# Performance work log

Measured on AMD Instinct MI355X. Metric: run time of the kernel, lower is better.

Reference implementation:

```python
import jax, jax.numpy as jnp
import numpy as np

B, N, C, H = 2, 2048, 1024, 16
D = C // H
EPS = 1e-5  # torch LayerNorm default


def layernorm(x, gamma, beta):
    mu = jnp.mean(x, axis=-1, keepdims=True)
    var = jnp.mean(jnp.square(x - mu), axis=-1, keepdims=True)
    return (x - mu) * jax.lax.rsqrt(var + EPS) * gamma + beta


def setup_inputs() -> dict:
    key = jax.random.key(0)
    ks = jax.random.split(key, 4)
    x = jax.random.normal(ks[0], (B, N, C), dtype=jnp.float32)
    w_qkv = jax.random.normal(ks[1], (3 * C, C), dtype=jnp.float32) * (C ** -0.5)
    w_proj = jax.random.normal(ks[2], (C, C), dtype=jnp.float32) * (C ** -0.5)
    return {
        "x": x,
        "w_qkv": w_qkv,
        "q_gamma": jnp.ones((C,), jnp.float32),
        "q_beta": jnp.zeros((C,), jnp.float32),
        "k_gamma": jnp.ones((C,), jnp.float32),
        "k_beta": jnp.zeros((C,), jnp.float32),
        "lpe_w": jnp.ones((C,), jnp.float32),
        "lpe_b": jnp.zeros((C,), jnp.float32),
        "w_proj": w_proj,
        "b_proj": jnp.zeros((C,), jnp.float32),
    }


def reference(x, w_qkv, q_gamma, q_beta, k_gamma, k_beta, lpe_w, lpe_b, w_proj, b_proj):
    b, n, c = x.shape
    scale = D ** -0.5
    qkv = jnp.einsum('bnc,fc->bnf', x, w_qkv)            # (B,N,3C)
    qkv = qkv.reshape(b, n, 3, H, D)
    q, k, v = qkv[:, :, 0], qkv[:, :, 1], qkv[:, :, 2]   # (B,N,H,D)
    # QK-norm: LayerNorm over flattened heads (dim C)
    q = layernorm(q.reshape(b, n, c), q_gamma, q_beta).reshape(b, n, H, D)
    k = layernorm(k.reshape(b, n, c), k_gamma, k_beta).reshape(b, n, H, D)
    # LPE: depthwise 1x1x1 conv == per-channel affine on v
    v_lpe = v.reshape(b, n, c) * lpe_w + lpe_b           # (B,N,C)
    # attention
    attn = jnp.einsum('bqhd,bkhd->bhqk', q * scale, k)   # (B,H,N,N)
    attn = jax.nn.softmax(attn, axis=-1)
    out = jnp.einsum('bhqk,bkhd->bqhd', attn, v).reshape(b, n, c)
    y = jnp.einsum('bnc,oc->bno', out + v_lpe, w_proj) + b_proj
    return y
```

## Files before the change

kernel.cpp:

```cpp
#include <hip/hip_runtime.h>
#include <stdint.h>

#define Bdim 2
#define Ndim 2048
#define Cdim 1024
#define Hdim 16
#define Ddim 64
#define Fdim 3072
#define Mdim 4096

typedef unsigned int  u32;
typedef unsigned short u16;
typedef float f32x4 __attribute__((ext_vector_type(4)));
typedef short s16x8 __attribute__((ext_vector_type(8)));
typedef unsigned short u16x4 __attribute__((ext_vector_type(4)));
typedef unsigned int u32x2 __attribute__((ext_vector_type(2)));

__device__ __forceinline__ u16 f2b(float f) {
  u32 u = __builtin_bit_cast(u32, f);
  u += 0x7FFFu + ((u >> 16) & 1u);
  return (u16)(u >> 16);
}
__device__ __forceinline__ float b2f(u16 h) {
  return __builtin_bit_cast(float, (u32)h << 16);
}
__device__ __forceinline__ u32 cvtpk(float a, float b) {
  u32 d;
  asm("v_cvt_pk_bf16_f32 %0, %1, %2" : "=v"(d) : "v"(a), "v"(b));
  return d;
}
__device__ __forceinline__ float rexp2(float x) { return __builtin_amdgcn_exp2f(x); }
__device__ __forceinline__ f32x4 mfma16(s16x8 a, s16x8 b, f32x4 c) {
  return __builtin_amdgcn_mfma_f32_16x16x32_bf16(a, b, c, 0, 0, 0);
}
__device__ __forceinline__ void gl_lds16(const void* g, void* l) {
  __builtin_amdgcn_global_load_lds(
      (const __attribute__((address_space(1))) void*)g,
      (__attribute__((address_space(3))) void*)l, 16, 0, 0);
}
__device__ __forceinline__ bool is_bf16(const void* qg) {
  return *(const u32*)qg == 0x3F803F80u;
}

__global__ __launch_bounds__(256)
void k_prep(const void* x, const void* wq, const void* wp,
            const void* g0, const void* g1, const void* g2, const void* g3,
            const void* g4, const void* g5, const void* g6,
            u16* xb, u16* wqb, u16* wpb, float* prm) {
  const int i = blockIdx.x * 256 + threadIdx.x;
  const bool isbf = is_bf16(g0);
  const void* src; u16* dst; int k;
  if (i < 1048576)      { src = x;  dst = xb;  k = i; }
  else if (i < 1835008) { src = wq; dst = wqb; k = i - 1048576; }
  else if (i < 2097152) { src = wp; dst = wpb; k = i - 1835008; }
  else {
    const int j = i - 2097152;
    if (j >= 1792) return;
    const int fi = j * 4;
    const int pi = fi >> 10, off = fi & 1023;
    const void* s = (pi == 0) ? g0 : (pi == 1) ? g1 : (pi == 2) ? g2
                  : (pi == 3) ? g3 : (pi == 4) ? g4 : (pi == 5) ? g5 : g6;
    float4 v;
    if (isbf) {
      u16x4 h = *(const u16x4*)((const u16*)s + off);
      v.x = b2f(h.x); v.y = b2f(h.y); v.z = b2f(h.z); v.w = b2f(h.w);
    } else {
      v = *(const float4*)((const float*)s + off);
    }
    *(float4*)(prm + fi) = v;
    return;
  }
  if (isbf) {
    ((u16x4*)dst)[k] = ((const u16x4*)src)[k];
  } else {
    float4 v = ((const float4*)src)[k];
    u16x4 o;
    o.x = f2b(v.x); o.y = f2b(v.y); o.z = f2b(v.z); o.w = f2b(v.w);
    ((u16x4*)dst)[k] = o;
  }
}

__global__ __launch_bounds__(256)
void k_gemm_qkv(const u16* __restrict__ A, const u16* __restrict__ W,
                u16* __restrict__ Cb, u16* __restrict__ vTp,
                int Msz, int Nsz, int Ksz) {
  __shared__ __align__(16) char lds[32768];
  const int tid = threadIdx.x;
  const int lane = tid & 63;
  const int wm = (tid >> 6) >> 1, wn = (tid >> 6) & 1;
  const int g = lane >> 4, cl = lane & 15;
  const int nwg = gridDim.x * gridDim.y;
  const int lid = blockIdx.y * gridDim.x + blockIdx.x;
  const int cpx = nwg >> 3;
  const int swz = (lid & 7) * cpx + (lid >> 3);
  const int row0 = (swz / gridDim.x) * 128, col0 = (swz % gridDim.x) * 128;
  const int KT = Ksz >> 5;

  f32x4 acc[4][4] = {};

  auto stage = [&](int buf, int kt) {
    const int k0 = kt << 5;
#pragma unroll
    for (int iss = 0; iss < 2; ++iss) {
      const int t = iss * 256 + tid;
      const int r = t >> 2;
      const int ss = (t & 3) ^ ((r >> 1) & 3);
      gl_lds16(A + (size_t)(row0 + r) * Ksz + k0 + ss * 8, &lds[buf * 16384 + t * 16]);
      gl_lds16(W + (size_t)(col0 + r) * Ksz + k0 + ss * 8, &lds[buf * 16384 + 8192 + t * 16]);
    }
  };

  stage(0, 0);
  __syncthreads();
  int cur = 0;
  for (int kt = 0; kt < KT; ++kt) {
    if (kt + 1 < KT) stage(cur ^ 1, kt + 1);
    const char* Ab = &lds[cur * 16384];
    const char* Bb = &lds[cur * 16384 + 8192];
    s16x8 af[4], bfr[4];
#pragma unroll
    for (int mi = 0; mi < 4; ++mi) {
      const int r = wm * 64 + mi * 16 + cl;
      const int s = g ^ ((r >> 1) & 3);
      af[mi] = *(const s16x8*)(Ab + r * 64 + s * 16);
    }
#pragma unroll
    for (int nj = 0; nj < 4; ++nj) {
      const int r = wn * 64 + nj * 16 + cl;
      const int s = g ^ ((r >> 1) & 3);
      bfr[nj] = *(const s16x8*)(Bb + r * 64 + s * 16);
    }
#pragma unroll
    for (int mi = 0; mi < 4; ++mi)
#pragma unroll
      for (int nj = 0; nj < 4; ++nj)
        acc[mi][nj] = mfma16(af[mi], bfr[nj], acc[mi][nj]);
    __syncthreads();
    cur ^= 1;
  }

#pragma unroll
  for (int mi = 0; mi < 4; ++mi)
#pragma unroll
    for (int nj = 0; nj < 4; ++nj) {
      const int m0 = row0 + wm * 64 + mi * 16 + g * 4;
      const int nbase = col0 + wn * 64 + nj * 16;
      const int n = nbase + cl;
      if (nbase >= 2048) {
        const int h = (nbase - 2048) >> 6;
        const int d = ((nbase - 2048) & 63) + cl;
        u16x4 pk;
#pragma unroll
        for (int r = 0; r < 4; ++r) pk[r] = f2b(acc[mi][nj][r]);
        *(u16x4*)(vTp + (size_t)h * (64 * 4096) + (size_t)d * 4096 + m0) = pk;
      } else {
#pragma unroll
        for (int r = 0; r < 4; ++r)
          Cb[(size_t)(m0 + r) * Nsz + n] = f2b(acc[mi][nj][r]);
      }
    }
}

__global__ __launch_bounds__(256)
void k_gemm_n64(const u16* __restrict__ A, const u16* __restrict__ W,
                void* __restrict__ Cout, const float* __restrict__ bias,
                const void* __restrict__ qg) {
  __shared__ __align__(16) char lds[24576];
  const int tid = threadIdx.x;
  const int lane = tid & 63;
  const int w = tid >> 6;
  const int g = lane >> 4, cl = lane & 15;
  const int nwg = gridDim.x * gridDim.y;
  const int lid = blockIdx.y * gridDim.x + blockIdx.x;
  const int cpx = nwg >> 3;
  const int swz = (lid & 7) * cpx + (lid >> 3);
  const int row0 = (swz / gridDim.x) * 128, col0 = (swz % gridDim.x) * 64;
  const int KT = Cdim >> 5;

  f32x4 acc[2][4] = {};

  auto stage = [&](int buf, int kt) {
    const int k0 = kt << 5;
#pragma unroll
    for (int iss = 0; iss < 2; ++iss) {
      const int t = iss * 256 + tid;
      const int r = t >> 2;
      const int ss = (t & 3) ^ ((r >> 1) & 3);
      gl_lds16(A + (size_t)(row0 + r) * Cdim + k0 + ss * 8, &lds[buf * 12288 + t * 16]);
    }
    {
      const int r = tid >> 2;
      const int ss = (tid & 3) ^ ((r >> 1) & 3);
      gl_lds16(W + (size_t)(col0 + r) * Cdim + k0 + ss * 8, &lds[buf * 12288 + 8192 + tid * 16]);
    }
  };

  stage(0, 0);
  __syncthreads();
  int cur = 0;
  for (int kt = 0; kt < KT; ++kt) {
    if (kt + 1 < KT) stage(cur ^ 1, kt + 1);
    const char* Ab = &lds[cur * 12288];
    const char* Bb = &lds[cur * 12288 + 8192];
    s16x8 af[2], bfr[4];
#pragma unroll
    for (int mi = 0; mi < 2; ++mi) {
      const int r = w * 32 + mi * 16 + cl;
      const int s = g ^ ((r >> 1) & 3);
      af[mi] = *(const s16x8*)(Ab + r * 64 + s * 16);
    }
#pragma unroll
    for (int nj = 0; nj < 4; ++nj) {
      const int r = nj * 16 + cl;
      const int s = g ^ ((r >> 1) & 3);
      bfr[nj] = *(const s16x8*)(Bb + r * 64 + s * 16);
    }
#pragma unroll
    for (int mi = 0; mi < 2; ++mi)
#pragma unroll
      for (int nj = 0; nj < 4; ++nj)
        acc[mi][nj] = mfma16(af[mi], bfr[nj], acc[mi][nj]);
    __syncthreads();
    cur ^= 1;
  }

  const u32 oflag = is_bf16(qg) ? 1u : 0u;
#pragma unroll
  for (int mi = 0; mi < 2; ++mi)
#pragma unroll
    for (int nj = 0; nj < 4; ++nj) {
      const int m0 = row0 + w * 32 + mi * 16 + g * 4;
      const int n = col0 + nj * 16 + cl;
#pragma unroll
      for (int r = 0; r < 4; ++r) {
        float v = acc[mi][nj][r] + bias[n];
        if (oflag) ((u16*)Cout)[(size_t)(m0 + r) * Cdim + n] = f2b(v);
        else       ((float*)Cout)[(size_t)(m0 + r) * Cdim + n] = v;
      }
    }
}

__global__ __launch_bounds__(256)
void k_ln(u16* __restrict__ qkv, const float* __restrict__ prm) {
  const int m = blockIdx.x;
  const int tid = threadIdx.x;
  const int lane = tid & 63, wv = tid >> 6;
  __shared__ float red[2][4];
  u16* row = qkv + (size_t)m * Fdim;
#pragma unroll
  for (int seg = 0; seg < 2; ++seg) {
    u16* s = row + seg * 1024;
    u16x4 v = *(const u16x4*)(s + tid * 4);
    float x0 = b2f(v.x), x1 = b2f(v.y), x2 = b2f(v.z), x3 = b2f(v.w);
    float sum = x0 + x1 + x2 + x3;
    float ssq = x0 * x0 + x1 * x1 + x2 * x2 + x3 * x3;
#pragma unroll
    for (int off = 32; off >= 1; off >>= 1) {
      sum += __shfl_xor(sum, off);
      ssq += __shfl_xor(ssq, off);
    }
    if (lane == 0) { red[0][wv] = sum; red[1][wv] = ssq; }
    __syncthreads();
    const float ts = red[0][0] + red[0][1] + red[0][2] + red[0][3];
    const float tq = red[1][0] + red[1][1] + red[1][2] + red[1][3];
    __syncthreads();
    const float mu = ts * (1.0f / 1024.0f);
    const float var = tq * (1.0f / 1024.0f) - mu * mu;
    const float rstd = rsqrtf(var + 1e-5f);
    const float scl = (seg == 0) ? (0.125f * 1.4426950408889634f) : 1.0f;
    const float* gam = prm + seg * 2048;
    const float* bet = prm + seg * 2048 + 1024;
    const int c = tid * 4;
    u16x4 o;
    o.x = f2b(((x0 - mu) * rstd * gam[c + 0] + bet[c + 0]) * scl);
    o.y = f2b(((x1 - mu) * rstd * gam[c + 1] + bet[c + 1]) * scl);
    o.z = f2b(((x2 - mu) * rstd * gam[c + 2] + bet[c + 2]) * scl);
    o.w = f2b(((x3 - mu) * rstd * gam[c + 3] + bet[c + 3]) * scl);
    *(u16x4*)(s + tid * 4) = o;
  }
}

__global__ __launch_bounds__(256, 3)
void k_attn(const u16* __restrict__ qkv, const u16* __restrict__ vT,
            u16* __restrict__ pin, const float* __restrict__ prm) {
  const int bid = blockIdx.x;
  const int qt = (bid >> 3) & 15;
  const int bh = (bid & 7) * 4 + (bid >> 7);
  const int b = bh >> 4, h = bh & 15;
  const int tid = threadIdx.x, lane = tid & 63, w = tid >> 6;
  const int g = lane >> 4, cl = lane & 15;
  const int c7 = cl & 7;
  const int mrow0 = b * Ndim + qt * 128;
  const int NT = Ndim / 64;

  const u16* Qg  = qkv + (size_t)mrow0 * Fdim + h * 64;
  const u16* Kg  = qkv + (size_t)(b * Ndim) * Fdim + Cdim + h * 64;
  const u16* vTg = vT + (size_t)h * (64 * 4096) + b * Ndim;

  __shared__ __align__(16) char klds[2][8192];
  __shared__ __align__(16) char vlds[2][8192];
  __shared__ __align__(16) char plds[4][4096];

  s16x8 bq[2][2];
#pragma unroll
  for (int qb = 0; qb < 2; ++qb)
#pragma unroll
    for (int kc = 0; kc < 2; ++kc)
      bq[qb][kc] = *(const s16x8*)(Qg + (size_t)(w * 32 + qb * 16 + cl) * Fdim + kc * 32 + g * 8);

  f32x4 o[2][4] = {};
  float mr[2] = {-1e30f, -1e30f};
  float lr[2] = {0.f, 0.f};

  const char* akp0 = &klds[0][cl * 128 + (((0 + g) ^ c7) << 4)];
  const char* akp1 = &klds[0][cl * 128 + (((4 + g) ^ c7) << 4)];
  const char* avp0 = &vlds[0][cl * 128 + (((0 + g) ^ c7) << 4)];
  const char* avp1 = &vlds[0][cl * 128 + (((4 + g) ^ c7) << 4)];
  char* pwp[4];
#pragma unroll
  for (int nj = 0; nj < 4; ++nj)
    pwp[nj] = &plds[w][cl * 128 + ((nj * 32 + g * 8) ^ (c7 << 4))];
  const char* bpp0 = &plds[w][cl * 128 + ((0  + g * 16) ^ (c7 << 4))];
  const char* bpp1 = &plds[w][cl * 128 + ((64 + g * 16) ^ (c7 << 4))];

  const int r0 = tid >> 3;
  const int ss0 = ((tid & 7) ^ (r0 & 7)) * 8;
  const u16* kp = Kg + (size_t)r0 * Fdim + ss0;
  const u16* vp = vTg + (size_t)r0 * 4096 + ss0;
  char* kd = &klds[0][tid * 16];
  char* vd = &vlds[0][tid * 16];

  gl_lds16(kp, kd);
  gl_lds16(kp + (size_t)32 * Fdim, kd + 4096);
  gl_lds16(vp, vd);
  gl_lds16(vp + (size_t)32 * 4096, vd + 4096);
  kp += (size_t)64 * Fdim;
  vp += 64;

#define ATTN_TILE(BUF, PREFETCH)                                              \
  {                                                                           \
               \
    asm volatile("s_waitcnt vmcnt(2)" ::: "memory");                          \
    __builtin_amdgcn_s_barrier();                                             \
    __builtin_amdgcn_sched_barrier(0);                                        \
    if (PREFETCH) {                                                           \
      gl_lds16(kp, kd + ((BUF) ^ 1) * 8192);                                  \
      gl_lds16(kp + (size_t)32 * Fdim, kd + ((BUF) ^ 1) * 8192 + 4096);       \
      gl_lds16(vp, vd + ((BUF) ^ 1) * 8192);                                  \
      gl_lds16(vp + (size_t)32 * 4096, vd + ((BUF) ^ 1) * 8192 + 4096);       \
      kp += (size_t)64 * Fdim;                                                \
      vp += 64;                                                               \
    }                                                                         \
    s16x8 ak[4][2];                                                           \
    _Pragma("unroll") for (int nj = 0; nj < 4; ++nj) {                        \
      ak[nj][0] = *(const s16x8*)(akp0 + (BUF) * 8192 + nj * 2048);           \
      ak[nj][1] = *(const s16x8*)(akp1 + (BUF) * 8192 + nj * 2048);           \
    }                                                                         \
                       \
    f32x4 sv[2][4];                                                           \
    __builtin_amdgcn_s_setprio(1);                                            \
    _Pragma("unroll") for (int qb = 0; qb < 2; ++qb)                          \
      _Pragma("unroll") for (int nj = 0; nj < 4; ++nj) {                      \
        f32x4 z = {0.f, 0.f, 0.f, 0.f};                                       \
        z = mfma16(ak[nj][0], bq[qb][0], z);                                  \
        z = mfma16(ak[nj][1], bq[qb][1], z);                                  \
        sv[qb][nj] = z;                                                       \
      }                                                                       \
    __builtin_amdgcn_s_setprio(0);                                            \
    _Pragma("unroll") for (int qb = 0; qb < 2; ++qb) {                        \
      float a0 = fmaxf(fmaxf(sv[qb][0][0], sv[qb][0][1]), sv[qb][0][2]);      \
      float a1 = fmaxf(fmaxf(sv[qb][0][3], sv[qb][1][0]), sv[qb][1][1]);      \
      float a2 = fmaxf(fmaxf(sv[qb][1][2], sv[qb][1][3]), sv[qb][2][0]);      \
      float a3 = fmaxf(fmaxf(sv[qb][2][1], sv[qb][2][2]), sv[qb][2][3]);      \
      float a4 = fmaxf(fmaxf(sv[qb][3][0], sv[qb][3][1]), sv[qb][3][2]);      \
      float b0v = fmaxf(fmaxf(a0, a1), a2);                                   \
      float b1v = fmaxf(fmaxf(a3, a4), sv[qb][3][3]);                         \
      float mx = fmaxf(b0v, b1v);                                             \
      if (!__all(mx <= mr[qb] + 7.0f)) {                                      \
        mx = fmaxf(mx, __shfl_xor(mx, 16));                                   \
        mx = fmaxf(mx, __shfl_xor(mx, 32));                                   \
        const float mn = fmaxf(mr[qb], mx);                                   \
        const float corr = rexp2(mr[qb] - mn);                                \
        mr[qb] = mn;                                                          \
        lr[qb] *= corr;                                                       \
        o[qb][0] *= corr; o[qb][1] *= corr;                                   \
        o[qb][2] *= corr; o[qb][3] *= corr;                                   \
      }                                                                       \
      const float mrq = mr[qb];                                               \
      float ssum = 0.f;                                                       \
      _Pragma("unroll") for (int nj = 0; nj < 4; ++nj) {                      \
        const float p0 = rexp2(sv[qb][nj][0] - mrq);                          \
        const float p1 = rexp2(sv[qb][nj][1] - mrq);                          \
        const float p2 = rexp2(sv[qb][nj][2] - mrq);                          \
        const float p3 = rexp2(sv[qb][nj][3] - mrq);                          \
        ssum += (p0 + p1) + (p2 + p3);                                        \
        u32x2 pk2;                                                            \
        pk2.x = cvtpk(p0, p1);                                                \
        pk2.y = cvtpk(p2, p3);                                                \
        *(u32x2*)(pwp[nj] + qb * 2048) = pk2;                                 \
      }                                                                       \
      lr[qb] += ssum;                                                         \
    }                                                                         \
           \
    if (PREFETCH) {                                                           \
      asm volatile("s_waitcnt vmcnt(4) lgkmcnt(0)" ::: "memory");             \
    } else {                                                                  \
      asm volatile("s_waitcnt vmcnt(0) lgkmcnt(0)" ::: "memory");             \
    }                                                                         \
    __builtin_amdgcn_s_barrier();                                             \
    __builtin_amdgcn_sched_barrier(0);                                        \
    s16x8 av[4][2];                                                           \
    _Pragma("unroll") for (int dc = 0; dc < 4; ++dc) {                        \
      av[dc][0] = *(const s16x8*)(avp0 + (BUF) * 8192 + dc * 2048);           \
      av[dc][1] = *(const s16x8*)(avp1 + (BUF) * 8192 + dc * 2048);           \
    }                                                                         \
    _Pragma("unroll") for (int qb = 0; qb < 2; ++qb) {                        \
      const s16x8 bp0 = *(const s16x8*)(bpp0 + qb * 2048);                    \
      const s16x8 bp1 = *(const s16x8*)(bpp1 + qb * 2048);                    \
      __builtin_amdgcn_s_setprio(1);                                          \
      _Pragma("unroll") for (int dc = 0; dc < 4; ++dc) {                      \
        o[qb][dc] = mfma16(av[dc][0], bp0, o[qb][dc]);                        \
        o[qb][dc] = mfma16(av[dc][1], bp1, o[qb][dc]);                        \
      }                                                                       \
      __builtin_amdgcn_s_setprio(0);                                          \
    }                                                                         \
  }

  for (int t = 0; t < NT; t += 2) {
    ATTN_TILE(0, true);
    ATTN_TILE(1, (t + 2 < NT));
  }
#undef ATTN_TILE

#pragma unroll
  for (int qb = 0; qb < 2; ++qb) {
    const int q = w * 32 + qb * 16 + cl;
    const int m = mrow0 + q;
    const int nseq = qt * 128 + q;
    float lt = lr[qb];
    lt += __shfl_xor(lt, 16);
    lt += __shfl_xor(lt, 32);
    const float inv = 1.0f / lt;
#pragma unroll
    for (int dc = 0; dc < 4; ++dc) {
      const int d0 = dc * 16 + g * 4;
      const int c = h * 64 + d0;
      const float4 lw = *(const float4*)(prm + 4096 + c);
      const float4 lb = *(const float4*)(prm + 5120 + c);
      float vr[4];
#pragma unroll
      for (int r = 0; r < 4; ++r) {
        const float vv = b2f(vTg[(size_t)(d0 + r) * 4096 + nseq]);
        vr[r] = o[qb][dc][r] * inv + vv * (&lw.x)[r] + (&lb.x)[r];
      }
      u32x2 ov;
      ov.x = cvtpk(vr[0], vr[1]);
      ov.y = cvtpk(vr[2], vr[3]);
      *(u32x2*)(pin + (size_t)m * Cdim + c) = ov;
    }
  }
}

extern "C" void kernel_launch(void* const* d_in, const int* in_sizes, int n_in,
                              void* d_out, int out_size, void* d_ws, size_t ws_size,
                              hipStream_t stream) {
  (void)in_sizes; (void)n_in; (void)out_size; (void)ws_size;
  char* ws = (char*)d_ws;
  float* prm    = (float*)(ws + 256);
  u16*   xb     = (u16*)(ws + 32768);
  u16*   wqkvb  = (u16*)(ws + 32768 + 8388608);
  u16*   wprojb = (u16*)(ws + 32768 + 8388608 + 6291456);
  u16*   qkv    = (u16*)(ws + 32768 + 8388608 + 6291456 + 2097152);
  u16*   vT     = (u16*)(ws + 32768 + 8388608 + 6291456 + 2097152 + 25165824);
  u16*   pin    = xb;

  k_prep<<<8199, 256, 0, stream>>>(d_in[0], d_in[1], d_in[8],
                                   d_in[2], d_in[3], d_in[4], d_in[5],
                                   d_in[6], d_in[7], d_in[9],
                                   xb, wqkvb, wprojb, prm);

  k_gemm_qkv<<<dim3(Fdim / 128, Mdim / 128), 256, 0, stream>>>(
      xb, wqkvb, qkv, vT, Mdim, Fdim, Cdim);

  k_ln<<<Mdim, 256, 0, stream>>>(qkv, prm);

  k_attn<<<dim3(512), 256, 0, stream>>>(qkv, vT, pin, prm);

  k_gemm_n64<<<dim3(Cdim / 64, Mdim / 128), 256, 0, stream>>>(
      pin, wprojb, d_out, prm + 6144, d_in[2]);
}
```

Measured before the change: 130.5 us.

## Deepen K/V LDS pipeline to four buffers and drop mid-tile barrier

Expands the K and V shared-memory ring from two to four buffers so loads are issued two tiles ahead. The mid-tile vmcnt wait and barrier before the PV stage become a plain lgkmcnt wait. Launch bounds drop from 3 to 2 blocks per SM to make room for the larger LDS footprint. This trades occupancy for deeper latency hiding and fewer barriers. Removing the barrier risks P buffer hazards, but plds is per-wave, so it is likely still safe.

```diff
diff --git a/kernel.cpp b/kernel.cpp
--- a/kernel.cpp
+++ b/kernel.cpp
@@ -280,7 +280,7 @@
   }
 }
 
-__global__ __launch_bounds__(256, 3)
+__global__ __launch_bounds__(256, 2)
 void k_attn(const u16* __restrict__ qkv, const u16* __restrict__ vT,
             u16* __restrict__ pin, const float* __restrict__ prm) {
   const int bid = blockIdx.x;
@@ -297,8 +297,8 @@
   const u16* Kg  = qkv + (size_t)(b * Ndim) * Fdim + Cdim + h * 64;
   const u16* vTg = vT + (size_t)h * (64 * 4096) + b * Ndim;
 
-  __shared__ __align__(16) char klds[2][8192];
-  __shared__ __align__(16) char vlds[2][8192];
+  __shared__ __align__(16) char klds[4][8192];
+  __shared__ __align__(16) char vlds[4][8192];
   __shared__ __align__(16) char plds[4][4096];
 
   s16x8 bq[2][2];
@@ -330,24 +330,28 @@
   char* kd = &klds[0][tid * 16];
   char* vd = &vlds[0][tid * 16];
 
-  gl_lds16(kp, kd);
-  gl_lds16(kp + (size_t)32 * Fdim, kd + 4096);
-  gl_lds16(vp, vd);
-  gl_lds16(vp + (size_t)32 * 4096, vd + 4096);
-  kp += (size_t)64 * Fdim;
-  vp += 64;
-
-#define ATTN_TILE(BUF, PREFETCH)                                              \
+#pragma unroll
+  for (int pt = 0; pt < 2; ++pt) {
+    gl_lds16(kp, kd + pt * 8192);
+    gl_lds16(kp + (size_t)32 * Fdim, kd + pt * 8192 + 4096);
+    gl_lds16(vp, vd + pt * 8192);
+    gl_lds16(vp + (size_t)32 * 4096, vd + pt * 8192 + 4096);
+    kp += (size_t)64 * Fdim;
+    vp += 64;
+  }
+
+#define ATTN_BODY(BUF, PRE, WAITINSN)                                         \
   {                                                                           \
-               \
-    asm volatile("s_waitcnt vmcnt(2)" ::: "memory");                          \
+    asm volatile(WAITINSN ::: "memory");                                      \
     __builtin_amdgcn_s_barrier();                                             \
     __builtin_amdgcn_sched_barrier(0);                                        \
-    if (PREFETCH) {                                                           \
-      gl_lds16(kp, kd + ((BUF) ^ 1) * 8192);                                  \
-      gl_lds16(kp + (size_t)32 * Fdim, kd + ((BUF) ^ 1) * 8192 + 4096);       \
-      gl_lds16(vp, vd + ((BUF) ^ 1) * 8192);                                  \
-      gl_lds16(vp + (size_t)32 * 4096, vd + ((BUF) ^ 1) * 8192 + 4096);       \
+    if (PRE) {                                                                \
+      char* kdd = kd + ((((BUF) + 2) & 3) * 8192);                            \
+      char* vdd = vd + ((((BUF) + 2) & 3) * 8192);                            \
+      gl_lds16(kp, kdd);                                                      \
+      gl_lds16(kp + (size_t)32 * Fdim, kdd + 4096);                           \
+      gl_lds16(vp, vdd);                                                      \
+      gl_lds16(vp + (size_t)32 * 4096, vdd + 4096);                           \
       kp += (size_t)64 * Fdim;                                                \
       vp += 64;                                                               \
     }                                                                         \
@@ -401,13 +405,8 @@
       }                                                                       \
       lr[qb] += ssum;                                                         \
     }                                                                         \
-           \
-    if (PREFETCH) {                                                           \
-      asm volatile("s_waitcnt vmcnt(4) lgkmcnt(0)" ::: "memory");             \
-    } else {                                                                  \
-      asm volatile("s_waitcnt vmcnt(0) lgkmcnt(0)" ::: "memory");             \
-    }                                                                         \
-    __builtin_amdgcn_s_barrier();                                             \
+                  \
+    asm volatile("s_waitcnt lgkmcnt(0)" ::: "memory");                        \
     __builtin_amdgcn_sched_barrier(0);                                        \
     s16x8 av[4][2];                                                           \
     _Pragma("unroll") for (int dc = 0; dc < 4; ++dc) {                        \
@@ -426,11 +425,17 @@
     }                                                                         \
   }
 
-  for (int t = 0; t < NT; t += 2) {
-    ATTN_TILE(0, true);
-    ATTN_TILE(1, (t + 2 < NT));
-  }
-#undef ATTN_TILE
+  for (int t = 0; t + 4 < NT; t += 4) {
+    ATTN_BODY(0, true, "s_waitcnt vmcnt(4)");
+    ATTN_BODY(1, true, "s_waitcnt vmcnt(4)");
+    ATTN_BODY(2, true, "s_waitcnt vmcnt(4)");
+    ATTN_BODY(3, true, "s_waitcnt vmcnt(4)");
+  }
+  ATTN_BODY(0, true,  "s_waitcnt vmcnt(4)");
+  ATTN_BODY(1, true,  "s_waitcnt vmcnt(4)");
+  ATTN_BODY(2, false, "s_waitcnt vmcnt(4)");
+  ATTN_BODY(3, false, "s_waitcnt vmcnt(0)");
+#undef ATTN_BODY
 
 #pragma unroll
   for (int qb = 0; qb < 2; ++qb) {
```

Measured after the change: 126.7 us. 1.03x faster.
